# Kernel tuning notes

Measured on AMD Instinct MI355X. Metric: run time of the kernel, lower is better.

## Reference

```python
import jax, jax.numpy as jnp
import numpy as np

VOCAB, D_IN, D_H, D_OUT, B, S = 32000, 512, 1024, 2, 16, 512

def _lstm_layer(x_seq, W_i, b_i, W_f, b_f, W_g, b_g, W_o, b_o):
    # x_seq: [B, S, D]; weights: [(D+H), H]
    Bsz = x_seq.shape[0]
    H0 = jnp.zeros((Bsz, D_H), x_seq.dtype)
    C0 = jnp.zeros((Bsz, D_H), x_seq.dtype)
    xs = jnp.swapaxes(x_seq, 0, 1)  # [S, B, D]
    def step(carry, x_t):
        H, C = carry
        comb = jnp.concatenate([x_t, H], axis=1)  # [B, D+H]
        I = jax.nn.sigmoid(comb @ W_i + b_i)
        F = jax.nn.sigmoid(comb @ W_f + b_f)
        G = jnp.tanh(comb @ W_g + b_g)
        O = jax.nn.sigmoid(comb @ W_o + b_o)
        C = F * C + I * G
        H = O * jnp.tanh(C)
        return (H, C), H
    (_, _), outs = jax.lax.scan(step, (H0, C0), xs)
    return jnp.swapaxes(outs, 0, 1)  # [B, S, H]

def setup_inputs() -> dict:
    key = jax.random.key(0)
    ks = jax.random.split(key, 20)
    tokens = jax.random.randint(ks[0], (B, S), 0, VOCAB)
    emb = jax.random.normal(ks[1], (VOCAB, D_IN), jnp.float32) * 0.02
    def gate(k, d_in):
        k1, k2 = jax.random.split(k)
        lim = 1.0 / np.sqrt(d_in + D_H)
        W = jax.random.uniform(k1, (d_in + D_H, D_H), jnp.float32, -lim, lim)
        b = jax.random.uniform(k2, (D_H,), jnp.float32, -lim, lim)
        return W, b
    inp = {"tokens": tokens, "emb": emb}
    for li, d_in in enumerate([D_IN, D_H]):
        for gi, g in enumerate("ifgo"):
            W, b = gate(ks[2 + li * 4 + gi], d_in)
            inp[f"W{li}_{g}"] = W
            inp[f"b{li}_{g}"] = b
        # fc head
    limf = 1.0 / np.sqrt(D_H)
    inp["Wfc"] = jax.random.uniform(ks[12], (D_H, D_OUT), jnp.float32, -limf, limf)
    inp["bfc"] = jax.random.uniform(ks[13], (D_OUT,), jnp.float32, -limf, limf)
    return inp

def reference(tokens, emb, W0_i, b0_i, W0_f, b0_f, W0_g, b0_g, W0_o, b0_o,
              W1_i, b1_i, W1_f, b1_f, W1_g, b1_g, W1_o, b1_o, Wfc, bfc):
    x = emb[tokens]  # [B, S, D_IN]
    x = _lstm_layer(x, W0_i, b0_i, W0_f, b0_f, W0_g, b0_g, W0_o, b0_o)
    x = _lstm_layer(x, W1_i, b1_i, W1_f, b1_f, W1_g, b1_g, W1_o, b1_o)
    logits = x @ Wfc + bfc  # [B, S, D_OUT]
    return jax.nn.log_softmax(logits, axis=-1)
```

## Files before the change

kernel.cpp:

```cpp
#include <hip/hip_runtime.h>
#include <math.h>


#define BB    16
#define SLEN  512
#define DH    1024
#define NBLK0 64

typedef __attribute__((ext_vector_type(8))) short short8;
typedef __attribute__((ext_vector_type(4))) float f32x4;

__device__ inline unsigned short f2bfbits(float x) {
  union { float f; unsigned u; } v; v.f = x;
  unsigned r = v.u + 0x7FFF + ((v.u >> 16) & 1);
  return (unsigned short)(r >> 16);
}

__global__ void zero_cnt_kernel(unsigned* cnt) {
  if (threadIdx.x < 128) cnt[threadIdx.x] = 0;
}

__global__ __launch_bounds__(256) void embed_kernel(const int* __restrict__ tokens,
                                                    const float* __restrict__ emb,
                                                    float* __restrict__ x0) {
  int idx = blockIdx.x * 256 + threadIdx.x;
  int r = idx >> 7, d4 = idx & 127;
  int tok = tokens[r];
  const float4* src = (const float4*)emb + (((size_t)tok) << 7) + d4;
  ((float4*)x0)[(((size_t)r) << 7) + d4] = *src;
}

__global__ __launch_bounds__(256) void xproj_kernel(
    const float* __restrict__ A, int K,
    const float* __restrict__ Wi, const float* __restrict__ Wf,
    const float* __restrict__ Wg, const float* __restrict__ Wo,
    const float* __restrict__ bi, const float* __restrict__ bf,
    const float* __restrict__ bg, const float* __restrict__ bo,
    float* __restrict__ Cout)
{
  __shared__ float As[8][128];
  __shared__ float Bs[8][128];
  const int tid = threadIdx.x;
  const int bn = blockIdx.x;
  const int bm = blockIdx.y;
  const int m0 = bm * 128;
  const int n0 = bn * 128;
  const int g = n0 >> 10;
  const float* W    = (g == 0) ? Wi : (g == 1) ? Wf : (g == 2) ? Wg : Wo;
  const float* bias = (g == 0) ? bi : (g == 1) ? bf : (g == 2) ? bg : bo;
  const int col0 = n0 & 1023;
  const int tx = tid & 15, ty = tid >> 4;
  const int lr = tid >> 1, lh = tid & 1;
  const int lk = tid >> 5, ln = (tid & 31) << 2;

  float acc[8][8];
#pragma unroll
  for (int i = 0; i < 8; ++i)
#pragma unroll
    for (int j = 0; j < 8; ++j) acc[i][j] = 0.f;

  for (int k0 = 0; k0 < K; k0 += 8) {
    float4 av = *(const float4*)(A + (size_t)(m0 + lr) * K + k0 + lh * 4);
    float4 bv = *(const float4*)(W + (size_t)(k0 + lk) * 1024 + col0 + ln);
    As[lh * 4 + 0][lr] = av.x;
    As[lh * 4 + 1][lr] = av.y;
    As[lh * 4 + 2][lr] = av.z;
    As[lh * 4 + 3][lr] = av.w;
    *(float4*)&Bs[lk][ln] = bv;
    __syncthreads();
#pragma unroll
    for (int p = 0; p < 8; ++p) {
      float a[8], b[8];
      *(float4*)&a[0] = *(const float4*)&As[p][ty * 8];
      *(float4*)&a[4] = *(const float4*)&As[p][ty * 8 + 4];
      *(float4*)&b[0] = *(const float4*)&Bs[p][tx * 4];
      *(float4*)&b[4] = *(const float4*)&Bs[p][64 + tx * 4];
#pragma unroll
      for (int i = 0; i < 8; ++i)
#pragma unroll
        for (int j = 0; j < 8; ++j) acc[i][j] += a[i] * b[j];
    }
    __syncthreads();
  }
  float4 bA = *(const float4*)(bias + col0 + tx * 4);
  float4 bB = *(const float4*)(bias + col0 + 64 + tx * 4);
#pragma unroll
  for (int i = 0; i < 8; ++i) {
    int m = m0 + ty * 8 + i;
    float* crow = Cout + (((size_t)m) << 12) + n0;
    float4 o1 = make_float4(acc[i][0] + bA.x, acc[i][1] + bA.y, acc[i][2] + bA.z, acc[i][3] + bA.w);
    float4 o2 = make_float4(acc[i][4] + bB.x, acc[i][5] + bB.y, acc[i][6] + bB.z, acc[i][7] + bB.w);
    *(float4*)(crow + tx * 4) = o1;
    *(float4*)(crow + 64 + tx * 4) = o2;
  }
}

__global__ __launch_bounds__(512, 2) void lstm_pipe(
    const float* __restrict__ xp,
    const float* __restrict__ W0i, const float* __restrict__ W0f,
    const float* __restrict__ W0g, const float* __restrict__ W0o,
    const float* __restrict__ W1i, const float* __restrict__ W1f,
    const float* __restrict__ W1g, const float* __restrict__ W1o,
    const float* __restrict__ b1i, const float* __restrict__ b1f,
    const float* __restrict__ b1g, const float* __restrict__ b1o,
    const float* __restrict__ Wfc,
    short* __restrict__ h0b16,
    short* __restrict__ h1b16,
    float2* __restrict__ part,
    unsigned* __restrict__ flags)
{
  __shared__ float Pre[8][16][17];
  const int tid  = threadIdx.x;
  const int wv   = tid >> 6;
  const int g    = wv & 3;
  const int kh   = wv >> 2;
  const int lane = tid & 63;
  const int q    = lane >> 4;
  const int n    = lane & 15;
  const int cb   = tid >> 4, cc = tid & 15;

  if (blockIdx.x < NBLK0) {
    const int c0 = blockIdx.x << 4;
    const float* Wsel = (g == 0) ? W0i : (g == 1) ? W0f : (g == 2) ? W0g : W0o;
    short8 wfrag[16];
#pragma unroll
    for (int kk = 0; kk < 16; ++kk)
#pragma unroll
      for (int j = 0; j < 8; ++j)
        wfrag[kk][j] = (short)f2bfbits(
            Wsel[(size_t)(512 + kh * 512 + kk * 32 + q * 8 + j) * 1024 + c0 + n]);

    float Creg = 0.f;
    const float* xpb = xp + ((size_t)g << 10) + c0 + n;
    f32x4 xpn = {0.f, 0.f, 0.f, 0.f};
    if (kh == 0) {
#pragma unroll
      for (int r = 0; r < 4; ++r)
        xpn[r] = xpb[((size_t)((q * 4 + r) * SLEN)) << 12];
    }

    for (int t = 0; t < SLEN; ++t) {
      f32x4 acc = (kh == 0) ? xpn : f32x4{0.f, 0.f, 0.f, 0.f};
      f32x4 acc2 = {0.f, 0.f, 0.f, 0.f};
      if (kh == 0 && t + 1 < SLEN) {
#pragma unroll
        for (int r = 0; r < 4; ++r)
          xpn[r] = xpb[((size_t)((q * 4 + r) * SLEN + t + 1)) << 12];
      }
      if (t > 0) {
        const short* hrow = h0b16 + (((size_t)(t - 1)) << 14) + n * 1024 + kh * 512 + q * 8;
#pragma unroll
        for (int kk = 0; kk < 16; kk += 2) {
          short8 a0 = *(const short8*)(hrow + kk * 32);
          short8 a1 = *(const short8*)(hrow + kk * 32 + 32);
          acc  = __builtin_amdgcn_mfma_f32_16x16x32_bf16(a0, wfrag[kk],     acc,  0, 0, 0);
          acc2 = __builtin_amdgcn_mfma_f32_16x16x32_bf16(a1, wfrag[kk + 1], acc2, 0, 0, 0);
        }
#pragma unroll
        for (int r = 0; r < 4; ++r) acc[r] += acc2[r];
      }
#pragma unroll
      for (int r = 0; r < 4; ++r) Pre[wv][q * 4 + r][n] = acc[r];
      __syncthreads();

      if (tid < 256) {
        float pI = Pre[0][cb][cc] + Pre[4][cb][cc];
        float pF = Pre[1][cb][cc] + Pre[5][cb][cc];
        float pG = Pre[2][cb][cc] + Pre[6][cb][cc];
        float pO = Pre[3][cb][cc] + Pre[7][cb][cc];
        float gI = 1.f / (1.f + __expf(-pI));
        float gF = 1.f / (1.f + __expf(-pF));
        float gG = tanhf(pG);
        float gO = 1.f / (1.f + __expf(-pO));
        Creg = gF * Creg + gI * gG;
        float h = gO * tanhf(Creg);

        unsigned mybits = (unsigned)f2bfbits(h);
        unsigned nbbits = (unsigned)__shfl_xor((int)mybits, 1, 64);
        if ((cc & 1) == 0) {
          unsigned pk = mybits | (nbbits << 16);
          __hip_atomic_store((unsigned*)(h0b16 + (((size_t)(t * 16 + cb)) << 10) + c0 + cc), pk,
                             __ATOMIC_RELAXED, __HIP_MEMORY_SCOPE_AGENT);
        }
      }
      __syncthreads();

      if (tid == 0)
        __hip_atomic_store(&flags[blockIdx.x], (unsigned)(t + 1),
                           __ATOMIC_RELAXED, __HIP_MEMORY_SCOPE_AGENT);
      if (t + 1 < SLEN) {
        if (tid < 64) {
          const unsigned tgt = (unsigned)(t + 1);
          while (true) {
            unsigned v0 = __hip_atomic_load(&flags[tid], __ATOMIC_RELAXED,
                                            __HIP_MEMORY_SCOPE_AGENT);
            if (__all((int)(v0 >= tgt))) break;
            __builtin_amdgcn_s_sleep(1);
          }
        }
        __syncthreads();
      }
    }
  } else {
    const int blk1 = blockIdx.x - NBLK0;
    const int c0 = blk1 << 4;
    const float* Wsel = (g == 0) ? W1i : (g == 1) ? W1f : (g == 2) ? W1g : W1o;
    const float* bsel = (g == 0) ? b1i : (g == 1) ? b1f : (g == 2) ? b1g : b1o;
    short8 wfrag[32];
#pragma unroll
    for (int kk = 0; kk < 32; ++kk)
#pragma unroll
      for (int j = 0; j < 8; ++j)
        wfrag[kk][j] = (short)f2bfbits(
            Wsel[(size_t)(kh * 1024 + kk * 32 + q * 8 + j) * 1024 + c0 + n]);
    const float bcol = (kh == 0) ? bsel[c0 + n] : 0.f;
    const float wfc0 = Wfc[(c0 + cc) * 2 + 0];
    const float wfc1 = Wfc[(c0 + cc) * 2 + 1];
    float Creg = 0.f;

    for (int t = 0; t < SLEN; ++t) {
      if (tid < 64) {
        const unsigned tgt0 = (unsigned)(t + 1);
        const unsigned tgt1 = (unsigned)t;
        while (true) {
          unsigned v0 = __hip_atomic_load(&flags[tid], __ATOMIC_RELAXED,
                                          __HIP_MEMORY_SCOPE_AGENT);
          unsigned v1 = __hip_atomic_load(&flags[64 + tid], __ATOMIC_RELAXED,
                                          __HIP_MEMORY_SCOPE_AGENT);
          if (__all((int)(v0 >= tgt0 && v1 >= tgt1))) break;
          __builtin_amdgcn_s_sleep(1);
        }
      }
      __syncthreads();

      f32x4 acc, acc2 = {0.f, 0.f, 0.f, 0.f};
#pragma unroll
      for (int r = 0; r < 4; ++r) acc[r] = bcol;

      if (kh == 0) {
        const short* xrow = h0b16 + (((size_t)t) << 14) + n * 1024 + q * 8;
#pragma unroll
        for (int kk = 0; kk < 32; kk += 2) {
          short8 a0 = *(const short8*)(xrow + kk * 32);
          short8 a1 = *(const short8*)(xrow + kk * 32 + 32);
          acc  = __builtin_amdgcn_mfma_f32_16x16x32_bf16(a0, wfrag[kk],     acc,  0, 0, 0);
          acc2 = __builtin_amdgcn_mfma_f32_16x16x32_bf16(a1, wfrag[kk + 1], acc2, 0, 0, 0);
        }
      } else if (t > 0) {
        const short* hrow = h1b16 + (((size_t)(t - 1)) << 14) + n * 1024 + q * 8;
#pragma unroll
        for (int kk = 0; kk < 32; kk += 2) {
          short8 a0 = *(const short8*)(hrow + kk * 32);
          short8 a1 = *(const short8*)(hrow + kk * 32 + 32);
          acc  = __builtin_amdgcn_mfma_f32_16x16x32_bf16(a0, wfrag[kk],     acc,  0, 0, 0);
          acc2 = __builtin_amdgcn_mfma_f32_16x16x32_bf16(a1, wfrag[kk + 1], acc2, 0, 0, 0);
        }
      }
#pragma unroll
      for (int r = 0; r < 4; ++r) acc[r] += acc2[r];

#pragma unroll
      for (int r = 0; r < 4; ++r) Pre[wv][q * 4 + r][n] = acc[r];
      __syncthreads();

      if (tid < 256) {
        float pI = Pre[0][cb][cc] + Pre[4][cb][cc];
        float pF = Pre[1][cb][cc] + Pre[5][cb][cc];
        float pG = Pre[2][cb][cc] + Pre[6][cb][cc];
        float pO = Pre[3][cb][cc] + Pre[7][cb][cc];
        float gI = 1.f / (1.f + __expf(-pI));
        float gF = 1.f / (1.f + __expf(-pF));
        float gG = tanhf(pG);
        float gO = 1.f / (1.f + __expf(-pO));
        Creg = gF * Creg + gI * gG;
        float h = gO * tanhf(Creg);

        float p0 = h * wfc0, p1 = h * wfc1;
#pragma unroll
        for (int m = 1; m < 16; m <<= 1) {
          p0 += __shfl_xor(p0, m, 64);
          p1 += __shfl_xor(p1, m, 64);
        }
        if (cc == 0)
          part[(size_t)(cb * SLEN + t) * 64 + blk1] = make_float2(p0, p1);

        unsigned mybits = (unsigned)f2bfbits(h);
        unsigned nbbits = (unsigned)__shfl_xor((int)mybits, 1, 64);
        if ((cc & 1) == 0) {
          unsigned pk = mybits | (nbbits << 16);
          __hip_atomic_store((unsigned*)(h1b16 + (((size_t)(t * 16 + cb)) << 10) + c0 + cc), pk,
                             __ATOMIC_RELAXED, __HIP_MEMORY_SCOPE_AGENT);
        }
      }
      __syncthreads();

      if (tid == 0)
        __hip_atomic_store(&flags[64 + blk1], (unsigned)(t + 1),
                           __ATOMIC_RELAXED, __HIP_MEMORY_SCOPE_AGENT);
    }
  }
}

__global__ __launch_bounds__(256) void finalize_kernel(const float2* __restrict__ part,
                                                       const float* __restrict__ bfc,
                                                       float* __restrict__ out)
{
  const int lane = threadIdx.x & 63;
  const int row = blockIdx.x * 4 + (threadIdx.x >> 6);
  float2 v = part[(size_t)row * 64 + lane];
  float s0 = v.x, s1 = v.y;
#pragma unroll
  for (int off = 32; off > 0; off >>= 1) {
    s0 += __shfl_down(s0, off);
    s1 += __shfl_down(s1, off);
  }
  if (lane == 0) {
    s0 += bfc[0];
    s1 += bfc[1];
    float m = fmaxf(s0, s1);
    float lse = m + logf(expf(s0 - m) + expf(s1 - m));
    out[((size_t)row << 1) + 0] = s0 - lse;
    out[((size_t)row << 1) + 1] = s1 - lse;
  }
}

extern "C" void kernel_launch(void* const* d_in, const int* in_sizes, int n_in,
                              void* d_out, int out_size, void* d_ws, size_t ws_size,
                              hipStream_t stream)
{
  const int*   tokens = (const int*)d_in[0];
  const float* emb = (const float*)d_in[1];
  const float* W0i = (const float*)d_in[2];
  const float* b0i = (const float*)d_in[3];
  const float* W0f = (const float*)d_in[4];
  const float* b0f = (const float*)d_in[5];
  const float* W0g = (const float*)d_in[6];
  const float* b0g = (const float*)d_in[7];
  const float* W0o = (const float*)d_in[8];
  const float* b0o = (const float*)d_in[9];
  const float* W1i = (const float*)d_in[10];
  const float* b1i = (const float*)d_in[11];
  const float* W1f = (const float*)d_in[12];
  const float* b1f = (const float*)d_in[13];
  const float* W1g = (const float*)d_in[14];
  const float* b1g = (const float*)d_in[15];
  const float* W1o = (const float*)d_in[16];
  const float* b1o = (const float*)d_in[17];
  const float* Wfc = (const float*)d_in[18];
  const float* bfc = (const float*)d_in[19];
  float* out = (float*)d_out;

  float* ws = (float*)d_ws;
  float* x0 = ws;
  float* hA = x0 + (size_t)8192 * 512;
  float* xp = hA + (size_t)8192 * 1024;
  unsigned* flags = (unsigned*)(xp + (size_t)8192 * 4096);
  short*  h0b16 = (short*)x0;
  short*  h1b16 = (short*)hA;
  float2* part  = (float2*)(hA + (size_t)8192 * 512);

  zero_cnt_kernel<<<1, 128, 0, stream>>>(flags);
  embed_kernel<<<4096, 256, 0, stream>>>(tokens, emb, x0);
  xproj_kernel<<<dim3(32, 64), 256, 0, stream>>>(x0, 512, W0i, W0f, W0g, W0o,
                                                 b0i, b0f, b0g, b0o, xp);
  lstm_pipe<<<128, 512, 0, stream>>>(xp,
                                     W0i, W0f, W0g, W0o,
                                     W1i, W1f, W1g, W1o,
                                     b1i, b1f, b1g, b1o,
                                     Wfc, h0b16, h1b16, part, flags);
  finalize_kernel<<<2048, 256, 0, stream>>>(part, bfc, out);
}
```

Before: 5.850 ms.

## Pin LSTM layers to single XCDs and offload layer-1 input projection to helper blocks

Blocks read their XCC ID from a hardware register and claim roles dynamically. Layer 0 and layer 1 recurrence each run on 64 blocks co-located on one XCD, which lets them use cheaper sc0 (XCD-local L2) flag and data stores and polling, with a watchdog fallback to agent-scope flags. 256 extra blocks compute layer 1's input projection from h0 ahead of time into a bf16 xp1 buffer, so layer 1's recurrent step does only a K=1024 matmul instead of 2048. The cost is many more launched blocks, extra helper synchronisation, bf16 rounding of the projected inputs, and reliance on co-residency and XCC placement behaviour that is not guaranteed.

```diff
diff --git a/kernel.cpp b/kernel.cpp
--- a/kernel.cpp
+++ b/kernel.cpp
@@ -2,10 +2,20 @@
 #include <math.h>
 
 
-#define BB    16
 #define SLEN  512
-#define DH    1024
-#define NBLK0 64
+#define HWREG_XCC_ID ((31 << 11) | (0 << 6) | 20)
+
+#define C_CNT0 0
+#define C_CNT1 1
+#define C_CNTF 2
+#define C_F0G  64
+#define C_F0L  128
+#define C_F1G  192
+#define C_F1L  256
+#define C_FF   512
+
+#define LOC_CAP 2048
+#define WD_CAP  65536
 
 typedef __attribute__((ext_vector_type(8))) short short8;
 typedef __attribute__((ext_vector_type(4))) float f32x4;
@@ -16,8 +26,25 @@
   return (unsigned short)(r >> 16);
 }
 
+__device__ inline unsigned ld_sc0(const unsigned* p) {
+  unsigned v;
+  asm volatile("global_load_dword %0, %1, off sc0\n\ts_waitcnt vmcnt(0)"
+               : "=v"(v) : "v"(p) : "memory");
+  return v;
+}
+__device__ inline void st_sc0(unsigned* p, unsigned v) {
+  asm volatile("global_store_dword %0, %1, off sc0" :: "v"(p), "v"(v) : "memory");
+}
+__device__ inline unsigned ld_ag(const unsigned* p) {
+  return __hip_atomic_load(p, __ATOMIC_RELAXED, __HIP_MEMORY_SCOPE_AGENT);
+}
+__device__ inline void st_ag(unsigned* p, unsigned v) {
+  __hip_atomic_store(p, v, __ATOMIC_RELAXED, __HIP_MEMORY_SCOPE_AGENT);
+}
+__device__ inline void cbar() { asm volatile("" ::: "memory"); }
+
 __global__ void zero_cnt_kernel(unsigned* cnt) {
-  if (threadIdx.x < 128) cnt[threadIdx.x] = 0;
+  cnt[threadIdx.x] = 0;
 }
 
 __global__ __launch_bounds__(256) void embed_kernel(const int* __restrict__ tokens,
@@ -95,8 +122,8 @@
   }
 }
 
-__global__ __launch_bounds__(512, 2) void lstm_pipe(
-    const float* __restrict__ xp,
+__global__ __launch_bounds__(512, 4) void lstm_pipe(
+    const float* xp,
     const float* __restrict__ W0i, const float* __restrict__ W0f,
     const float* __restrict__ W0g, const float* __restrict__ W0o,
     const float* __restrict__ W1i, const float* __restrict__ W1f,
@@ -104,12 +131,14 @@
     const float* __restrict__ b1i, const float* __restrict__ b1f,
     const float* __restrict__ b1g, const float* __restrict__ b1o,
     const float* __restrict__ Wfc,
-    short* __restrict__ h0b16,
-    short* __restrict__ h1b16,
+    short* __restrict__ h0,
+    short* __restrict__ h1,
+    unsigned short* xp1,
     float2* __restrict__ part,
-    unsigned* __restrict__ flags)
+    unsigned* __restrict__ ctl)
 {
   __shared__ float Pre[8][16][17];
+  __shared__ int s_role;
   const int tid  = threadIdx.x;
   const int wv   = tid >> 6;
   const int g    = wv & 3;
@@ -119,8 +148,39 @@
   const int n    = lane & 15;
   const int cb   = tid >> 4, cc = tid & 15;
 
-  if (blockIdx.x < NBLK0) {
-    const int c0 = blockIdx.x << 4;
+  unsigned* f0G = ctl + C_F0G;
+  unsigned* f0L = ctl + C_F0L;
+  unsigned* f1G = ctl + C_F1G;
+  unsigned* f1L = ctl + C_F1L;
+  unsigned* fF  = ctl + C_FF;
+
+  if (tid == 0) {
+    unsigned xid = (unsigned)__builtin_amdgcn_s_getreg(HWREG_XCC_ID) & 0xFu;
+    int role = -1;
+    unsigned tk;
+    if (xid == 0u)      { tk = atomicAdd(&ctl[C_CNT0], 1u); if (tk < 64u) role = (int)tk; }
+    else if (xid == 1u) { tk = atomicAdd(&ctl[C_CNT1], 1u); if (tk < 64u) role = 64 + (int)tk; }
+    if (role < 0) { tk = atomicAdd(&ctl[C_CNTF], 1u); if (tk < 256u) role = 128 + (int)tk; }
+    if (role < 0) {
+      int w = 0;
+      for (;;) {
+        if (ld_ag(&ctl[C_CNT0]) >= 64u && ld_ag(&ctl[C_CNT1]) >= 64u) break;
+        if (++w > 4096) break;
+        __builtin_amdgcn_s_sleep(8);
+      }
+      if (ld_ag(&ctl[C_CNT0]) < 64u) { tk = atomicAdd(&ctl[C_CNT0], 1u); if (tk < 64u) role = (int)tk; }
+      if (role < 0 && ld_ag(&ctl[C_CNT1]) < 64u) { tk = atomicAdd(&ctl[C_CNT1], 1u); if (tk < 64u) role = 64 + (int)tk; }
+    }
+    s_role = role;
+  }
+  __syncthreads();
+  const int role = s_role;
+  if (role < 0) return;
+
+  int use_loc = 1, broken = 0;
+
+  if (role < 64) {
+    const int rr = role, c0 = rr << 4;
     const float* Wsel = (g == 0) ? W0i : (g == 1) ? W0f : (g == 2) ? W0g : W0o;
     short8 wfrag[16];
 #pragma unroll
@@ -140,6 +200,20 @@
     }
 
     for (int t = 0; t < SLEN; ++t) {
+      if (t > 0 && !broken) {
+        const unsigned tgt = (unsigned)t;
+        if (use_loc) {
+          int it = 0;
+          for (;;) { unsigned v = ld_sc0(&f0L[lane]); if (__all((int)(v >= tgt))) break;
+                     if (++it > LOC_CAP) { use_loc = 0; break; } __builtin_amdgcn_s_sleep(1); }
+        }
+        if (!use_loc) {
+          int it = 0;
+          for (;;) { unsigned v = ld_ag(&f0G[lane]); if (__all((int)(v >= tgt))) break;
+                     if (++it > WD_CAP) { broken = 1; break; } __builtin_amdgcn_s_sleep(1); }
+        }
+        cbar();
+      }
       f32x4 acc = (kh == 0) ? xpn : f32x4{0.f, 0.f, 0.f, 0.f};
       f32x4 acc2 = {0.f, 0.f, 0.f, 0.f};
       if (kh == 0 && t + 1 < SLEN) {
@@ -148,7 +222,7 @@
           xpn[r] = xpb[((size_t)((q * 4 + r) * SLEN + t + 1)) << 12];
       }
       if (t > 0) {
-        const short* hrow = h0b16 + (((size_t)(t - 1)) << 14) + n * 1024 + kh * 512 + q * 8;
+        const short* hrow = h0 + (((size_t)(t - 1)) << 14) + n * 1024 + kh * 512 + q * 8;
 #pragma unroll
         for (int kk = 0; kk < 16; kk += 2) {
           short8 a0 = *(const short8*)(hrow + kk * 32);
@@ -179,86 +253,77 @@
         unsigned nbbits = (unsigned)__shfl_xor((int)mybits, 1, 64);
         if ((cc & 1) == 0) {
           unsigned pk = mybits | (nbbits << 16);
-          __hip_atomic_store((unsigned*)(h0b16 + (((size_t)(t * 16 + cb)) << 10) + c0 + cc), pk,
-                             __ATOMIC_RELAXED, __HIP_MEMORY_SCOPE_AGENT);
-        }
-      }
-      __syncthreads();
-
-      if (tid == 0)
-        __hip_atomic_store(&flags[blockIdx.x], (unsigned)(t + 1),
-                           __ATOMIC_RELAXED, __HIP_MEMORY_SCOPE_AGENT);
-      if (t + 1 < SLEN) {
-        if (tid < 64) {
-          const unsigned tgt = (unsigned)(t + 1);
-          while (true) {
-            unsigned v0 = __hip_atomic_load(&flags[tid], __ATOMIC_RELAXED,
-                                            __HIP_MEMORY_SCOPE_AGENT);
-            if (__all((int)(v0 >= tgt))) break;
-            __builtin_amdgcn_s_sleep(1);
-          }
-        }
-        __syncthreads();
-      }
-    }
-  } else {
-    const int blk1 = blockIdx.x - NBLK0;
-    const int c0 = blk1 << 4;
+          unsigned* addr = (unsigned*)(h0 + (((size_t)(t * 16 + cb)) << 10) + c0 + cc);
+          st_ag(addr, pk);
+          st_sc0(addr, pk);
+        }
+      }
+      asm volatile("s_waitcnt vmcnt(0)" ::: "memory");
+      __syncthreads();
+      if (tid == 0) {
+        st_ag(&f0G[rr], (unsigned)(t + 1));
+        st_sc0(&f0L[rr], (unsigned)(t + 1));
+      }
+    }
+  } else if (role < 128) {
+    const int rr = role - 64, c0 = rr << 4;
     const float* Wsel = (g == 0) ? W1i : (g == 1) ? W1f : (g == 2) ? W1g : W1o;
-    const float* bsel = (g == 0) ? b1i : (g == 1) ? b1f : (g == 2) ? b1g : b1o;
-    short8 wfrag[32];
-#pragma unroll
-    for (int kk = 0; kk < 32; ++kk)
+    short8 wfrag[16];
+#pragma unroll
+    for (int kk = 0; kk < 16; ++kk)
 #pragma unroll
       for (int j = 0; j < 8; ++j)
         wfrag[kk][j] = (short)f2bfbits(
-            Wsel[(size_t)(kh * 1024 + kk * 32 + q * 8 + j) * 1024 + c0 + n]);
-    const float bcol = (kh == 0) ? bsel[c0 + n] : 0.f;
+            Wsel[(size_t)(1024 + kh * 512 + kk * 32 + q * 8 + j) * 1024 + c0 + n]);
     const float wfc0 = Wfc[(c0 + cc) * 2 + 0];
     const float wfc1 = Wfc[(c0 + cc) * 2 + 1];
     float Creg = 0.f;
 
     for (int t = 0; t < SLEN; ++t) {
-      if (tid < 64) {
-        const unsigned tgt0 = (unsigned)(t + 1);
-        const unsigned tgt1 = (unsigned)t;
-        while (true) {
-          unsigned v0 = __hip_atomic_load(&flags[tid], __ATOMIC_RELAXED,
-                                          __HIP_MEMORY_SCOPE_AGENT);
-          unsigned v1 = __hip_atomic_load(&flags[64 + tid], __ATOMIC_RELAXED,
-                                          __HIP_MEMORY_SCOPE_AGENT);
-          if (__all((int)(v0 >= tgt0 && v1 >= tgt1))) break;
-          __builtin_amdgcn_s_sleep(1);
-        }
-      }
-      __syncthreads();
-
-      f32x4 acc, acc2 = {0.f, 0.f, 0.f, 0.f};
-#pragma unroll
-      for (int r = 0; r < 4; ++r) acc[r] = bcol;
-
+      if (!broken) {
+        const unsigned tgtF = (unsigned)(t >> 2) + 1u;
+        const unsigned base = ((unsigned)t & 3u) * 64u;
+        int it = 0;
+        for (;;) { unsigned v = ld_ag(&fF[base + lane]); if (__all((int)(v >= tgtF))) break;
+                   if (++it > WD_CAP) { broken = 1; break; } __builtin_amdgcn_s_sleep(1); }
+        cbar();
+      }
+      if (t > 0 && !broken) {
+        const unsigned tgt = (unsigned)t;
+        if (use_loc) {
+          int it = 0;
+          for (;;) { unsigned v = ld_sc0(&f1L[lane]); if (__all((int)(v >= tgt))) break;
+                     if (++it > LOC_CAP) { use_loc = 0; break; } __builtin_amdgcn_s_sleep(1); }
+        }
+        if (!use_loc) {
+          int it = 0;
+          for (;;) { unsigned v = ld_ag(&f1G[lane]); if (__all((int)(v >= tgt))) break;
+                     if (++it > WD_CAP) { broken = 1; break; } __builtin_amdgcn_s_sleep(1); }
+        }
+        cbar();
+      }
+
+      f32x4 acc = {0.f, 0.f, 0.f, 0.f};
+      f32x4 acc2 = {0.f, 0.f, 0.f, 0.f};
       if (kh == 0) {
-        const short* xrow = h0b16 + (((size_t)t) << 14) + n * 1024 + q * 8;
-#pragma unroll
-        for (int kk = 0; kk < 32; kk += 2) {
-          short8 a0 = *(const short8*)(xrow + kk * 32);
-          short8 a1 = *(const short8*)(xrow + kk * 32 + 32);
-          acc  = __builtin_amdgcn_mfma_f32_16x16x32_bf16(a0, wfrag[kk],     acc,  0, 0, 0);
-          acc2 = __builtin_amdgcn_mfma_f32_16x16x32_bf16(a1, wfrag[kk + 1], acc2, 0, 0, 0);
-        }
-      } else if (t > 0) {
-        const short* hrow = h1b16 + (((size_t)(t - 1)) << 14) + n * 1024 + q * 8;
-#pragma unroll
-        for (int kk = 0; kk < 32; kk += 2) {
+#pragma unroll
+        for (int r = 0; r < 4; ++r) {
+          unsigned u = (unsigned)xp1[(((size_t)((q * 4 + r) * SLEN + t)) << 13) + 4096 + (g << 10) + c0 + n] << 16;
+          acc[r] = __uint_as_float(u);
+        }
+      }
+      if (t > 0) {
+        const short* hrow = h1 + (((size_t)(t - 1)) << 14) + n * 1024 + kh * 512 + q * 8;
+#pragma unroll
+        for (int kk = 0; kk < 16; kk += 2) {
           short8 a0 = *(const short8*)(hrow + kk * 32);
           short8 a1 = *(const short8*)(hrow + kk * 32 + 32);
           acc  = __builtin_amdgcn_mfma_f32_16x16x32_bf16(a0, wfrag[kk],     acc,  0, 0, 0);
           acc2 = __builtin_amdgcn_mfma_f32_16x16x32_bf16(a1, wfrag[kk + 1], acc2, 0, 0, 0);
         }
-      }
-#pragma unroll
-      for (int r = 0; r < 4; ++r) acc[r] += acc2[r];
-
+#pragma unroll
+        for (int r = 0; r < 4; ++r) acc[r] += acc2[r];
+      }
 #pragma unroll
       for (int r = 0; r < 4; ++r) Pre[wv][q * 4 + r][n] = acc[r];
       __syncthreads();
@@ -282,21 +347,81 @@
           p1 += __shfl_xor(p1, m, 64);
         }
         if (cc == 0)
-          part[(size_t)(cb * SLEN + t) * 64 + blk1] = make_float2(p0, p1);
+          part[(size_t)(cb * SLEN + t) * 64 + rr] = make_float2(p0, p1);
 
         unsigned mybits = (unsigned)f2bfbits(h);
         unsigned nbbits = (unsigned)__shfl_xor((int)mybits, 1, 64);
         if ((cc & 1) == 0) {
           unsigned pk = mybits | (nbbits << 16);
-          __hip_atomic_store((unsigned*)(h1b16 + (((size_t)(t * 16 + cb)) << 10) + c0 + cc), pk,
-                             __ATOMIC_RELAXED, __HIP_MEMORY_SCOPE_AGENT);
-        }
-      }
-      __syncthreads();
-
-      if (tid == 0)
-        __hip_atomic_store(&flags[64 + blk1], (unsigned)(t + 1),
-                           __ATOMIC_RELAXED, __HIP_MEMORY_SCOPE_AGENT);
+          unsigned* addr = (unsigned*)(h1 + (((size_t)(t * 16 + cb)) << 10) + c0 + cc);
+          st_ag(addr, pk);
+          st_sc0(addr, pk);
+        }
+      }
+      asm volatile("s_waitcnt vmcnt(0)" ::: "memory");
+      __syncthreads();
+      if (tid == 0) {
+        st_ag(&f1G[rr], (unsigned)(t + 1));
+        st_sc0(&f1L[rr], (unsigned)(t + 1));
+      }
+    }
+  } else {
+    const int f = role - 128;
+    const int par = f >> 6;
+    const int c0f = (f & 63) << 4;
+    const float* Wsel = (g == 0) ? W1i : (g == 1) ? W1f : (g == 2) ? W1g : W1o;
+    short8 wfrag[16];
+#pragma unroll
+    for (int kk = 0; kk < 16; ++kk)
+#pragma unroll
+      for (int j = 0; j < 8; ++j)
+        wfrag[kk][j] = (short)f2bfbits(
+            Wsel[(size_t)(kh * 512 + kk * 32 + q * 8 + j) * 1024 + c0f + n]);
+    float bias4[4] = {0.f, 0.f, 0.f, 0.f};
+    if (tid < 256) {
+      bias4[0] = b1i[c0f + cc]; bias4[1] = b1f[c0f + cc];
+      bias4[2] = b1g[c0f + cc]; bias4[3] = b1o[c0f + cc];
+    }
+
+    for (int t = par; t < SLEN; t += 4) {
+      if (!broken) {
+        const unsigned tgt = (unsigned)(t + 1);
+        int it = 0;
+        for (;;) { unsigned v = ld_ag(&f0G[lane]); if (__all((int)(v >= tgt))) break;
+                   if (++it > WD_CAP) { broken = 1; break; } __builtin_amdgcn_s_sleep(2); }
+        cbar();
+      }
+      const short* xrow = h0 + (((size_t)t) << 14) + n * 1024 + kh * 512 + q * 8;
+      f32x4 acc = {0.f, 0.f, 0.f, 0.f};
+      f32x4 acc2 = {0.f, 0.f, 0.f, 0.f};
+#pragma unroll
+      for (int kk = 0; kk < 16; kk += 2) {
+        short8 a0 = *(const short8*)(xrow + kk * 32);
+        short8 a1 = *(const short8*)(xrow + kk * 32 + 32);
+        acc  = __builtin_amdgcn_mfma_f32_16x16x32_bf16(a0, wfrag[kk],     acc,  0, 0, 0);
+        acc2 = __builtin_amdgcn_mfma_f32_16x16x32_bf16(a1, wfrag[kk + 1], acc2, 0, 0, 0);
+      }
+#pragma unroll
+      for (int r = 0; r < 4; ++r) acc[r] += acc2[r];
+#pragma unroll
+      for (int r = 0; r < 4; ++r) Pre[wv][q * 4 + r][n] = acc[r];
+      __syncthreads();
+
+      if (tid < 256) {
+#pragma unroll
+        for (int g2 = 0; g2 < 4; ++g2) {
+          float pv = Pre[g2][cb][cc] + Pre[g2 + 4][cb][cc] + bias4[g2];
+          unsigned my = (unsigned)f2bfbits(pv);
+          unsigned nb = (unsigned)__shfl_xor((int)my, 1, 64);
+          if ((cc & 1) == 0) {
+            unsigned pk = my | (nb << 16);
+            st_ag((unsigned*)(xp1 + (((size_t)(cb * SLEN + t)) << 13) + 4096 + (g2 << 10) + c0f + cc), pk);
+          }
+        }
+      }
+      asm volatile("s_waitcnt vmcnt(0)" ::: "memory");
+      __syncthreads();
+      if (tid == 0) st_ag(&fF[f], (unsigned)(t >> 2) + 1u);
     }
   }
 }
@@ -354,19 +479,21 @@
   float* x0 = ws;
   float* hA = x0 + (size_t)8192 * 512;
   float* xp = hA + (size_t)8192 * 1024;
-  unsigned* flags = (unsigned*)(xp + (size_t)8192 * 4096);
-  short*  h0b16 = (short*)x0;
-  short*  h1b16 = (short*)hA;
-  float2* part  = (float2*)(hA + (size_t)8192 * 512);
-
-  zero_cnt_kernel<<<1, 128, 0, stream>>>(flags);
+  unsigned* ctl = (unsigned*)(xp + (size_t)8192 * 4096);
+
+  short*  h0   = (short*)x0;
+  short*  h1   = (short*)hA;
+  float2* part = (float2*)(hA + (size_t)8192 * 512);
+  unsigned short* xp1 = (unsigned short*)xp;
+
+  zero_cnt_kernel<<<1, 1024, 0, stream>>>(ctl);
   embed_kernel<<<4096, 256, 0, stream>>>(tokens, emb, x0);
   xproj_kernel<<<dim3(32, 64), 256, 0, stream>>>(x0, 512, W0i, W0f, W0g, W0o,
                                                  b0i, b0f, b0g, b0o, xp);
-  lstm_pipe<<<128, 512, 0, stream>>>(xp,
-                                     W0i, W0f, W0g, W0o,
-                                     W1i, W1f, W1g, W1o,
-                                     b1i, b1f, b1g, b1o,
-                                     Wfc, h0b16, h1b16, part, flags);
+  lstm_pipe<<<1024, 512, 0, stream>>>(xp,
+                                      W0i, W0f, W0g, W0o,
+                                      W1i, W1f, W1g, W1o,
+                                      b1i, b1f, b1g, b1o,
+                                      Wfc, h0, h1, xp1, part, ctl);
   finalize_kernel<<<2048, 256, 0, stream>>>(part, bfc, out);
 }
```

Measured after the change: 11.17 ms. 1.91x slower.

## Move input projection to bf16 MFMA and split layer-0/1 sync flags

Applied to the files above, without the earlier changes.

Replaces the fp32 SIMT input-projection GEMM with a bf16 MFMA kernel. The embedding is converted to bf16 and the layer-0 input weights are transposed to bf16 in a separate pre-pass. The pipelined LSTM kernel gets separate flag arrays for layer-0 to layer-0, layer-0 to layer-1 and layer-1 to layer-1 signalling. Layer-1 waves now wait only on the flags they need (kh==0 waves on layer 0, kh==1 waves on layer 1) and the block-wide barrier after the wait is removed. This cuts GEMM cost and the contention from polling shared flag cache lines, but adds bf16 rounding to the input projection and relies on per-wave waits without a block barrier.

```diff
diff --git a/kernel.cpp b/kernel.cpp
--- a/kernel.cpp
+++ b/kernel.cpp
@@ -2,10 +2,11 @@
 #include <math.h>
 
 
-#define BB    16
 #define SLEN  512
-#define DH    1024
-#define NBLK0 64
+
+#define C_F0A  64
+#define C_F0B  128
+#define C_F1   192
 
 typedef __attribute__((ext_vector_type(8))) short short8;
 typedef __attribute__((ext_vector_type(4))) float f32x4;
@@ -16,83 +17,94 @@
   return (unsigned short)(r >> 16);
 }
 
+__device__ inline unsigned ld_ag(const unsigned* p) {
+  return __hip_atomic_load(p, __ATOMIC_RELAXED, __HIP_MEMORY_SCOPE_AGENT);
+}
+__device__ inline void st_ag(unsigned* p, unsigned v) {
+  __hip_atomic_store(p, v, __ATOMIC_RELAXED, __HIP_MEMORY_SCOPE_AGENT);
+}
+
 __global__ void zero_cnt_kernel(unsigned* cnt) {
-  if (threadIdx.x < 128) cnt[threadIdx.x] = 0;
-}
-
-__global__ __launch_bounds__(256) void embed_kernel(const int* __restrict__ tokens,
-                                                    const float* __restrict__ emb,
-                                                    float* __restrict__ x0) {
+  cnt[threadIdx.x] = 0;
+}
+
+__global__ __launch_bounds__(256) void embed_bf16_kernel(const int* __restrict__ tokens,
+                                                         const float* __restrict__ emb,
+                                                         short* __restrict__ x0bf) {
   int idx = blockIdx.x * 256 + threadIdx.x;
-  int r = idx >> 7, d4 = idx & 127;
+  int r = idx >> 6, c8 = (idx & 63) << 3;
   int tok = tokens[r];
-  const float4* src = (const float4*)emb + (((size_t)tok) << 7) + d4;
-  ((float4*)x0)[(((size_t)r) << 7) + d4] = *src;
-}
-
-__global__ __launch_bounds__(256) void xproj_kernel(
-    const float* __restrict__ A, int K,
-    const float* __restrict__ Wi, const float* __restrict__ Wf,
-    const float* __restrict__ Wg, const float* __restrict__ Wo,
+  const float* src = emb + ((size_t)tok << 9) + c8;
+  float4 a = *(const float4*)(src);
+  float4 b = *(const float4*)(src + 4);
+  short8 o;
+  o[0] = (short)f2bfbits(a.x); o[1] = (short)f2bfbits(a.y);
+  o[2] = (short)f2bfbits(a.z); o[3] = (short)f2bfbits(a.w);
+  o[4] = (short)f2bfbits(b.x); o[5] = (short)f2bfbits(b.y);
+  o[6] = (short)f2bfbits(b.z); o[7] = (short)f2bfbits(b.w);
+  *(short8*)(x0bf + ((size_t)r << 9) + c8) = o;
+}
+
+__global__ __launch_bounds__(256) void wconv_kernel(const float* __restrict__ Wi,
+                                                    const float* __restrict__ Wf,
+                                                    const float* __restrict__ Wg,
+                                                    const float* __restrict__ Wo,
+                                                    short* __restrict__ Wt) {
+  int gid = blockIdx.x * 256 + threadIdx.x;
+  int gi = gid >> 16;
+  int rem = gid & 65535;
+  int col = rem >> 6;
+  int k8 = (rem & 63) << 3;
+  const float* W = (gi == 0) ? Wi : (gi == 1) ? Wf : (gi == 2) ? Wg : Wo;
+  short8 o;
+#pragma unroll
+  for (int j = 0; j < 8; ++j)
+    o[j] = (short)f2bfbits(W[(size_t)(k8 + j) * 1024 + col]);
+  *(short8*)(Wt + (((size_t)((gi << 10) + col)) << 9) + k8) = o;
+}
+
+__global__ __launch_bounds__(256) void xproj_mfma_kernel(
+    const short* __restrict__ x0bf,
+    const short* __restrict__ Wt,
     const float* __restrict__ bi, const float* __restrict__ bf,
     const float* __restrict__ bg, const float* __restrict__ bo,
-    float* __restrict__ Cout)
+    float* __restrict__ xp)
 {
-  __shared__ float As[8][128];
-  __shared__ float Bs[8][128];
   const int tid = threadIdx.x;
-  const int bn = blockIdx.x;
-  const int bm = blockIdx.y;
-  const int m0 = bm * 128;
-  const int n0 = bn * 128;
-  const int g = n0 >> 10;
-  const float* W    = (g == 0) ? Wi : (g == 1) ? Wf : (g == 2) ? Wg : Wo;
+  const int w = tid >> 6;
+  const int lane = tid & 63;
+  const int q = lane >> 4;
+  const int n = lane & 15;
+  const int cx = blockIdx.x;
+  const int g = cx >> 4;
+  const int cbase = ((cx & 15) << 6) + (w << 4);
+  const int m0 = blockIdx.y << 4;
   const float* bias = (g == 0) ? bi : (g == 1) ? bf : (g == 2) ? bg : bo;
-  const int col0 = n0 & 1023;
-  const int tx = tid & 15, ty = tid >> 4;
-  const int lr = tid >> 1, lh = tid & 1;
-  const int lk = tid >> 5, ln = (tid & 31) << 2;
-
-  float acc[8][8];
-#pragma unroll
-  for (int i = 0; i < 8; ++i)
-#pragma unroll
-    for (int j = 0; j < 8; ++j) acc[i][j] = 0.f;
-
-  for (int k0 = 0; k0 < K; k0 += 8) {
-    float4 av = *(const float4*)(A + (size_t)(m0 + lr) * K + k0 + lh * 4);
-    float4 bv = *(const float4*)(W + (size_t)(k0 + lk) * 1024 + col0 + ln);
-    As[lh * 4 + 0][lr] = av.x;
-    As[lh * 4 + 1][lr] = av.y;
-    As[lh * 4 + 2][lr] = av.z;
-    As[lh * 4 + 3][lr] = av.w;
-    *(float4*)&Bs[lk][ln] = bv;
-    __syncthreads();
-#pragma unroll
-    for (int p = 0; p < 8; ++p) {
-      float a[8], b[8];
-      *(float4*)&a[0] = *(const float4*)&As[p][ty * 8];
-      *(float4*)&a[4] = *(const float4*)&As[p][ty * 8 + 4];
-      *(float4*)&b[0] = *(const float4*)&Bs[p][tx * 4];
-      *(float4*)&b[4] = *(const float4*)&Bs[p][64 + tx * 4];
-#pragma unroll
-      for (int i = 0; i < 8; ++i)
-#pragma unroll
-        for (int j = 0; j < 8; ++j) acc[i][j] += a[i] * b[j];
-    }
-    __syncthreads();
+
+  const short* wp = Wt + (((size_t)((g << 10) + cbase + n)) << 9) + q * 8;
+  short8 wfrag[16];
+#pragma unroll
+  for (int kk = 0; kk < 16; ++kk) wfrag[kk] = *(const short8*)(wp + kk * 32);
+
+  const float bcol = bias[cbase + n];
+  f32x4 acc, acc2 = {0.f, 0.f, 0.f, 0.f};
+#pragma unroll
+  for (int r = 0; r < 4; ++r) acc[r] = bcol;
+
+  const short* ap = x0bf + (((size_t)(m0 + n)) << 9) + q * 8;
+#pragma unroll
+  for (int kk = 0; kk < 16; kk += 2) {
+    short8 a0 = *(const short8*)(ap + kk * 32);
+    short8 a1 = *(const short8*)(ap + kk * 32 + 32);
+    acc  = __builtin_amdgcn_mfma_f32_16x16x32_bf16(a0, wfrag[kk],     acc,  0, 0, 0);
+    acc2 = __builtin_amdgcn_mfma_f32_16x16x32_bf16(a1, wfrag[kk + 1], acc2, 0, 0, 0);
   }
-  float4 bA = *(const float4*)(bias + col0 + tx * 4);
-  float4 bB = *(const float4*)(bias + col0 + 64 + tx * 4);
-#pragma unroll
-  for (int i = 0; i < 8; ++i) {
-    int m = m0 + ty * 8 + i;
-    float* crow = Cout + (((size_t)m) << 12) + n0;
-    float4 o1 = make_float4(acc[i][0] + bA.x, acc[i][1] + bA.y, acc[i][2] + bA.z, acc[i][3] + bA.w);
-    float4 o2 = make_float4(acc[i][4] + bB.x, acc[i][5] + bB.y, acc[i][6] + bB.z, acc[i][7] + bB.w);
-    *(float4*)(crow + tx * 4) = o1;
-    *(float4*)(crow + 64 + tx * 4) = o2;
-  }
+#pragma unroll
+  for (int r = 0; r < 4; ++r) acc[r] += acc2[r];
+
+#pragma unroll
+  for (int r = 0; r < 4; ++r)
+    xp[(((size_t)(m0 + q * 4 + r)) << 12) + (g << 10) + cbase + n] = acc[r];
 }
 
 __global__ __launch_bounds__(512, 2) void lstm_pipe(
@@ -107,7 +119,7 @@
     short* __restrict__ h0b16,
     short* __restrict__ h1b16,
     float2* __restrict__ part,
-    unsigned* __restrict__ flags)
+    unsigned* __restrict__ ctl)
 {
   __shared__ float Pre[8][16][17];
   const int tid  = threadIdx.x;
@@ -119,8 +131,12 @@
   const int n    = lane & 15;
   const int cb   = tid >> 4, cc = tid & 15;
 
-  if (blockIdx.x < NBLK0) {
-    const int c0 = blockIdx.x << 4;
+  unsigned* f0a = ctl + C_F0A;
+  unsigned* f0b = ctl + C_F0B;
+  unsigned* f1  = ctl + C_F1;
+
+  if (blockIdx.x < 64) {
+    const int rr = blockIdx.x, c0 = rr << 4;
     const float* Wsel = (g == 0) ? W0i : (g == 1) ? W0f : (g == 2) ? W0g : W0o;
     short8 wfrag[16];
 #pragma unroll
@@ -179,21 +195,20 @@
         unsigned nbbits = (unsigned)__shfl_xor((int)mybits, 1, 64);
         if ((cc & 1) == 0) {
           unsigned pk = mybits | (nbbits << 16);
-          __hip_atomic_store((unsigned*)(h0b16 + (((size_t)(t * 16 + cb)) << 10) + c0 + cc), pk,
-                             __ATOMIC_RELAXED, __HIP_MEMORY_SCOPE_AGENT);
+          st_ag((unsigned*)(h0b16 + (((size_t)(t * 16 + cb)) << 10) + c0 + cc), pk);
         }
       }
       __syncthreads();
 
-      if (tid == 0)
-        __hip_atomic_store(&flags[blockIdx.x], (unsigned)(t + 1),
-                           __ATOMIC_RELAXED, __HIP_MEMORY_SCOPE_AGENT);
+      if (tid == 0) {
+        st_ag(&f0a[rr], (unsigned)(t + 1));
+        st_ag(&f0b[rr], (unsigned)(t + 1));
+      }
       if (t + 1 < SLEN) {
         if (tid < 64) {
           const unsigned tgt = (unsigned)(t + 1);
-          while (true) {
-            unsigned v0 = __hip_atomic_load(&flags[tid], __ATOMIC_RELAXED,
-                                            __HIP_MEMORY_SCOPE_AGENT);
+          for (;;) {
+            unsigned v0 = ld_ag(&f0a[tid]);
             if (__all((int)(v0 >= tgt))) break;
             __builtin_amdgcn_s_sleep(1);
           }
@@ -202,8 +217,7 @@
       }
     }
   } else {
-    const int blk1 = blockIdx.x - NBLK0;
-    const int c0 = blk1 << 4;
+    const int rr = blockIdx.x - 64, c0 = rr << 4;
     const float* Wsel = (g == 0) ? W1i : (g == 1) ? W1f : (g == 2) ? W1g : W1o;
     const float* bsel = (g == 0) ? b1i : (g == 1) ? b1f : (g == 2) ? b1g : b1o;
     short8 wfrag[32];
@@ -219,19 +233,21 @@
     float Creg = 0.f;
 
     for (int t = 0; t < SLEN; ++t) {
-      if (tid < 64) {
+      if (kh == 0) {
         const unsigned tgt0 = (unsigned)(t + 1);
+        for (;;) {
+          unsigned v0 = ld_ag(&f0b[lane]);
+          if (__all((int)(v0 >= tgt0))) break;
+          __builtin_amdgcn_s_sleep(1);
+        }
+      } else if (t > 0) {
         const unsigned tgt1 = (unsigned)t;
-        while (true) {
-          unsigned v0 = __hip_atomic_load(&flags[tid], __ATOMIC_RELAXED,
-                                          __HIP_MEMORY_SCOPE_AGENT);
-          unsigned v1 = __hip_atomic_load(&flags[64 + tid], __ATOMIC_RELAXED,
-                                          __HIP_MEMORY_SCOPE_AGENT);
-          if (__all((int)(v0 >= tgt0 && v1 >= tgt1))) break;
+        for (;;) {
+          unsigned v1 = ld_ag(&f1[lane]);
+          if (__all((int)(v1 >= tgt1))) break;
           __builtin_amdgcn_s_sleep(1);
         }
       }
-      __syncthreads();
 
       f32x4 acc, acc2 = {0.f, 0.f, 0.f, 0.f};
 #pragma unroll
@@ -282,21 +298,19 @@
           p1 += __shfl_xor(p1, m, 64);
         }
         if (cc == 0)
-          part[(size_t)(cb * SLEN + t) * 64 + blk1] = make_float2(p0, p1);
+          part[(size_t)(cb * SLEN + t) * 64 + rr] = make_float2(p0, p1);
 
         unsigned mybits = (unsigned)f2bfbits(h);
         unsigned nbbits = (unsigned)__shfl_xor((int)mybits, 1, 64);
         if ((cc & 1) == 0) {
           unsigned pk = mybits | (nbbits << 16);
-          __hip_atomic_store((unsigned*)(h1b16 + (((size_t)(t * 16 + cb)) << 10) + c0 + cc), pk,
-                             __ATOMIC_RELAXED, __HIP_MEMORY_SCOPE_AGENT);
+          st_ag((unsigned*)(h1b16 + (((size_t)(t * 16 + cb)) << 10) + c0 + cc), pk);
         }
       }
       __syncthreads();
 
       if (tid == 0)
-        __hip_atomic_store(&flags[64 + blk1], (unsigned)(t + 1),
-                           __ATOMIC_RELAXED, __HIP_MEMORY_SCOPE_AGENT);
+        st_ag(&f1[rr], (unsigned)(t + 1));
     }
   }
 }
@@ -354,19 +368,23 @@
   float* x0 = ws;
   float* hA = x0 + (size_t)8192 * 512;
   float* xp = hA + (size_t)8192 * 1024;
-  unsigned* flags = (unsigned*)(xp + (size_t)8192 * 4096);
-  short*  h0b16 = (short*)x0;
-  short*  h1b16 = (short*)hA;
-  float2* part  = (float2*)(hA + (size_t)8192 * 512);
-
-  zero_cnt_kernel<<<1, 128, 0, stream>>>(flags);
-  embed_kernel<<<4096, 256, 0, stream>>>(tokens, emb, x0);
-  xproj_kernel<<<dim3(32, 64), 256, 0, stream>>>(x0, 512, W0i, W0f, W0g, W0o,
-                                                 b0i, b0f, b0g, b0o, xp);
+  unsigned* ctl = (unsigned*)(xp + (size_t)8192 * 4096);
+
+  short*  x0bf = (short*)x0;
+  short*  h0   = (short*)x0;
+  short*  h1   = (short*)hA;
+  float2* part = (float2*)(hA + (size_t)8192 * 512);
+  short*  Wt   = (short*)(hA + (size_t)5 * 1024 * 1024);
+
+  zero_cnt_kernel<<<1, 256, 0, stream>>>(ctl);
+  embed_bf16_kernel<<<2048, 256, 0, stream>>>(tokens, emb, x0bf);
+  wconv_kernel<<<1024, 256, 0, stream>>>(W0i, W0f, W0g, W0o, Wt);
+  xproj_mfma_kernel<<<dim3(64, 512), 256, 0, stream>>>(x0bf, Wt,
+                                                       b0i, b0f, b0g, b0o, xp);
   lstm_pipe<<<128, 512, 0, stream>>>(xp,
                                      W0i, W0f, W0g, W0o,
                                      W1i, W1f, W1g, W1o,
                                      b1i, b1f, b1g, b1o,
-                                     Wfc, h0b16, h1b16, part, flags);
+                                     Wfc, h0, h1, part, ctl);
   finalize_kernel<<<2048, 256, 0, stream>>>(part, bfc, out);
 }
```

After: 5.626 ms. 3.8% less time.
